# Performance work log

Hardware: AMD Instinct MI355X
Metric: run time of the kernel (lower is better)

## Reference

```python
import jax, jax.numpy as jnp
import numpy as np

B, E, H, L, V = 128, 1024, 1024, 2, 32001  # vocab = output_size + 1
PAD_IDX = 1000


def gru_cell(x, h, w_ih, w_hh, b_ih, b_hh):
    # PyTorch GRU cell math; gates ordered (r, z, n)
    gi = x @ w_ih.T + b_ih            # [B, 3H]
    gh = h @ w_hh.T + b_hh            # [B, 3H]
    i_r, i_z, i_n = jnp.split(gi, 3, axis=-1)
    h_r, h_z, h_n = jnp.split(gh, 3, axis=-1)
    r = jax.nn.sigmoid(i_r + h_r)
    z = jax.nn.sigmoid(i_z + h_z)
    n = jnp.tanh(i_n + r * h_n)
    return (1.0 - z) * n + z * h


def setup_inputs() -> dict:
    key = jax.random.key(0)
    ks = jax.random.split(key, 16)
    input_vector = jax.random.randint(ks[0], (B,), 0, V)
    hidden = jax.random.normal(ks[1], (L, B, H), dtype=jnp.float32)
    emb = jax.random.uniform(ks[2], (V, E), minval=-0.1, maxval=0.1, dtype=jnp.float32)
    emb = emb.at[PAD_IDX].set(0.0)  # padding_idx
    s = 1.0 / np.sqrt(H)
    def u(k, shape):
        return jax.random.uniform(k, shape, minval=-s, maxval=s, dtype=jnp.float32)
    w_ih0 = u(ks[3], (3 * H, E)); w_hh0 = u(ks[4], (3 * H, H))
    b_ih0 = u(ks[5], (3 * H,));  b_hh0 = u(ks[6], (3 * H,))
    w_ih1 = u(ks[7], (3 * H, H)); w_hh1 = u(ks[8], (3 * H, H))
    b_ih1 = u(ks[9], (3 * H,));  b_hh1 = u(ks[10], (3 * H,))
    w_out = jax.random.uniform(ks[11], (V, H), minval=-0.1, maxval=0.1, dtype=jnp.float32)
    b_out = jnp.zeros((V,), dtype=jnp.float32)
    return dict(input_vector=input_vector, hidden=hidden, emb=emb,
                w_ih0=w_ih0, w_hh0=w_hh0, b_ih0=b_ih0, b_hh0=b_hh0,
                w_ih1=w_ih1, w_hh1=w_hh1, b_ih1=b_ih1, b_hh1=b_hh1,
                w_out=w_out, b_out=b_out)


def reference(input_vector, hidden, emb, w_ih0, w_hh0, b_ih0, b_hh0,
              w_ih1, w_hh1, b_ih1, b_hh1, w_out, b_out):
    x = jax.nn.relu(emb[input_vector])          # [B, E] (seq_len=1 squeezed)
    h0 = gru_cell(x, hidden[0], w_ih0, w_hh0, b_ih0, b_hh0)   # [B, H]
    h1 = gru_cell(h0, hidden[1], w_ih1, w_hh1, b_ih1, b_hh1)  # [B, H]
    logits = h1 @ w_out.T + b_out               # [B, V]
    out = jax.nn.log_softmax(logits, axis=-1)   # [B, V]
    hidden_out = jnp.stack([h0, h1], axis=0)    # [L, B, H]
    return out, hidden_out
```

## Files before the change

### kernel.cpp

```cpp
#include <hip/hip_runtime.h>
#include <cmath>

#define BATCH 128
#define KDIM 1024
#define VOCAB 32001
#define G3 3072
#define GIP_STRIDE (BATCH * G3)

typedef __bf16 bf16_t;
typedef bf16_t bf16x8 __attribute__((ext_vector_type(8)));
typedef float f32x4 __attribute__((ext_vector_type(4)));

__device__ __forceinline__ void stage16(const float* g, void* lds_wave_base) {
    __builtin_amdgcn_global_load_lds(
        (const __attribute__((address_space(1))) void*)g,
        (__attribute__((address_space(3))) void*)lds_wave_base, 16, 0, 0);
}

__device__ __forceinline__ bf16x8 frag_from_lds(const float* s, int row, int quad) {
    const int s7 = row & 7;
    const f32x4 u = *(const f32x4*)(s + row * 32 + (((2 * quad) ^ s7) * 4));
    const f32x4 v = *(const f32x4*)(s + row * 32 + (((2 * quad + 1) ^ s7) * 4));
    bf16x8 r;
    r[0] = (bf16_t)u[0]; r[1] = (bf16_t)u[1]; r[2] = (bf16_t)u[2]; r[3] = (bf16_t)u[3];
    r[4] = (bf16_t)v[0]; r[5] = (bf16_t)v[1]; r[6] = (bf16_t)v[2]; r[7] = (bf16_t)v[3];
    return r;
}

template<int BM, bool BIAS>
__device__ __forceinline__ void gemm_staged_core(
    const float* __restrict__ A, const float* __restrict__ W,
    float* __restrict__ C, const float* __restrict__ bias,
    int ldc, int Wrows, int m0, int n0, int kbeg, int kend)
{
    __shared__ float sA[BM * 32];
    __shared__ float sB[64 * 32];
    const int t    = threadIdx.x;
    const int wave = t >> 6;
    const int lane = t & 63;
    const int l15  = lane & 15;
    const int quad = lane >> 4;
    const int srow = t >> 3;
    const int sg   = t & 7;

    constexpr int MFRAG = BM / 16;
    f32x4 acc[MFRAG];
#pragma unroll
    for (int i = 0; i < MFRAG; ++i) acc[i] = f32x4{0.f, 0.f, 0.f, 0.f};

    for (int k0 = kbeg; k0 < kend; k0 += 32) {
#pragma unroll
        for (int r = 0; r < BM / 32; ++r) {
            const int row = r * 32 + srow;
            const int kg  = sg ^ (row & 7);
            stage16(A + (size_t)(m0 + row) * KDIM + k0 + kg * 4,
                    (char*)sA + r * 4096 + wave * 1024);
        }
#pragma unroll
        for (int r = 0; r < 2; ++r) {
            const int row = r * 32 + srow;
            int wr = n0 + row; if (wr > Wrows - 1) wr = Wrows - 1;
            const int kg = sg ^ (row & 7);
            stage16(W + (size_t)wr * KDIM + k0 + kg * 4,
                    (char*)sB + r * 4096 + wave * 1024);
        }
        __syncthreads();
        const bf16x8 bf = frag_from_lds(sB, wave * 16 + l15, quad);
#pragma unroll
        for (int i = 0; i < MFRAG; ++i) {
            const bf16x8 af = frag_from_lds(sA, i * 16 + l15, quad);
            acc[i] = __builtin_amdgcn_mfma_f32_16x16x32_bf16(af, bf, acc[i], 0, 0, 0);
        }
        __syncthreads();
    }

    const int col = n0 + wave * 16 + l15;
    if (col < Wrows) {
        const float bv = BIAS ? bias[col] : 0.f;
#pragma unroll
        for (int i = 0; i < MFRAG; ++i)
#pragma unroll
            for (int r = 0; r < 4; ++r) {
                const int row = m0 + i * 16 + quad * 4 + r;
                C[(size_t)row * ldc + col] = acc[i][r] + bv;
            }
    }
}

__global__ __launch_bounds__(256) void gemm_vocab(const float* __restrict__ A,
                                                  const float* __restrict__ W,
                                                  const float* __restrict__ bias,
                                                  float* __restrict__ C) {
    gemm_staged_core<64, true>(A, W, C, bias, VOCAB, VOCAB,
                               blockIdx.x * 64, blockIdx.y * 64, 0, KDIM);
}

__global__ __launch_bounds__(256) void gemm_gru(const float* __restrict__ x,
                                                const float* __restrict__ wih,
                                                float* __restrict__ giP,
                                                const float* __restrict__ h,
                                                const float* __restrict__ whh,
                                                float* __restrict__ ghP) {
    const int m0    = (blockIdx.x & 1) * 64;
    const int split = blockIdx.x >> 1;
    const int n0    = blockIdx.y * 64;
    const float* A; const float* W; float* C;
    if (blockIdx.z == 0) { A = x; W = wih; C = giP; }
    else                 { A = h; W = whh; C = ghP; }
    C += (size_t)split * GIP_STRIDE;
    gemm_staged_core<64, false>(A, W, C, nullptr, G3, G3, m0, n0,
                                split * 256, split * 256 + 256);
}

__global__ __launch_bounds__(256) void embed_relu(const int* __restrict__ idx,
                                                  const float* __restrict__ emb,
                                                  float* __restrict__ x) {
    const int i  = blockIdx.x * 256 + threadIdx.x;
    const int b  = i >> 8;
    const int e4 = i & 255;
    const f32x4 v = ((const f32x4*)(emb + (size_t)idx[b] * KDIM))[e4];
    f32x4 o;
#pragma unroll
    for (int k = 0; k < 4; ++k) o[k] = fmaxf(v[k], 0.f);
    ((f32x4*)x)[i] = o;
}

__device__ __forceinline__ f32x4 sum_splits(const float* p) {
    f32x4 s = *(const f32x4*)p;
    s += *(const f32x4*)(p + GIP_STRIDE);
    s += *(const f32x4*)(p + 2 * GIP_STRIDE);
    s += *(const f32x4*)(p + 3 * GIP_STRIDE);
    return s;
}

__global__ __launch_bounds__(256) void gru_gate(const float* __restrict__ giP,
                                                const float* __restrict__ ghP,
                                                const float* __restrict__ b_ih,
                                                const float* __restrict__ b_hh,
                                                const float* __restrict__ hprev,
                                                float* __restrict__ hout) {
    const int i  = blockIdx.x * 256 + threadIdx.x;
    const int b  = i >> 8;
    const int j  = (i & 255) * 4;
    const size_t base = (size_t)b * G3 + j;

    f32x4 ir = sum_splits(giP + base),        hr = sum_splits(ghP + base);
    f32x4 iz = sum_splits(giP + base + 1024), hz = sum_splits(ghP + base + 1024);
    f32x4 in = sum_splits(giP + base + 2048), hn = sum_splits(ghP + base + 2048);
    const f32x4 bir = *(const f32x4*)(b_ih + j);
    const f32x4 biz = *(const f32x4*)(b_ih + j + 1024);
    const f32x4 bin = *(const f32x4*)(b_ih + j + 2048);
    const f32x4 bhr = *(const f32x4*)(b_hh + j);
    const f32x4 bhz = *(const f32x4*)(b_hh + j + 1024);
    const f32x4 bhn = *(const f32x4*)(b_hh + j + 2048);
    const f32x4 hp  = *(const f32x4*)(hprev + (size_t)b * KDIM + j);

    f32x4 o;
#pragma unroll
    for (int k = 0; k < 4; ++k) {
        const float r = 1.f / (1.f + __expf(-(ir[k] + bir[k] + hr[k] + bhr[k])));
        const float z = 1.f / (1.f + __expf(-(iz[k] + biz[k] + hz[k] + bhz[k])));
        const float a = in[k] + bin[k] + r * (hn[k] + bhn[k]);
        const float n = 1.f - 2.f / (__expf(2.f * a) + 1.f);
        o[k] = (1.f - z) * n + z * hp[k];
    }
    *(f32x4*)(hout + (size_t)b * KDIM + j) = o;
}

__global__ __launch_bounds__(1024) void log_softmax_rows(float* __restrict__ out) {
    float* row = out + (size_t)blockIdx.x * VOCAB;
    const int t = threadIdx.x;
    __shared__ float sm[16], ss[16];

    float m = -3.4e38f, s = 0.f;
    for (int i = t; i < VOCAB; i += 1024) {
        const float v  = row[i];
        const float mn = fmaxf(m, v);
        s = s * __expf(m - mn) + __expf(v - mn);
        m = mn;
    }
#pragma unroll
    for (int o = 32; o; o >>= 1) {
        const float mo = __shfl_down(m, o);
        const float so = __shfl_down(s, o);
        const float mn = fmaxf(m, mo);
        s = s * __expf(m - mn) + so * __expf(mo - mn);
        m = mn;
    }
    if ((t & 63) == 0) { sm[t >> 6] = m; ss[t >> 6] = s; }
    __syncthreads();
    if (t == 0) {
        float M = sm[0], S = ss[0];
#pragma unroll
        for (int w = 1; w < 16; ++w) {
            const float mn = fmaxf(M, sm[w]);
            S = S * __expf(M - mn) + ss[w] * __expf(sm[w] - mn);
            M = mn;
        }
        sm[0] = M + __logf(S);
    }
    __syncthreads();
    const float L = sm[0];

    for (int i = t * 4; i + 3 < VOCAB; i += 4096) {
        f32x4 v = *(const f32x4*)(row + i);
        v[0] -= L; v[1] -= L; v[2] -= L; v[3] -= L;
        *(f32x4*)(row + i) = v;
    }
    if (t == 0) row[32000] -= L;
}

extern "C" void kernel_launch(void* const* d_in, const int* in_sizes, int n_in,
                              void* d_out, int out_size, void* d_ws, size_t ws_size,
                              hipStream_t stream) {
    const int*   ivec  = (const int*)  d_in[0];
    const float* hidden= (const float*)d_in[1];
    const float* emb   = (const float*)d_in[2];
    const float* w_ih0 = (const float*)d_in[3];
    const float* w_hh0 = (const float*)d_in[4];
    const float* b_ih0 = (const float*)d_in[5];
    const float* b_hh0 = (const float*)d_in[6];
    const float* w_ih1 = (const float*)d_in[7];
    const float* w_hh1 = (const float*)d_in[8];
    const float* b_ih1 = (const float*)d_in[9];
    const float* b_hh1 = (const float*)d_in[10];
    const float* w_out = (const float*)d_in[11];
    const float* b_out = (const float*)d_in[12];

    float* out = (float*)d_out;
    float* h0  = out + (size_t)BATCH * VOCAB;
    float* h1  = h0 + BATCH * KDIM;

    float* x   = out;
    float* giP = out + 131072;
    float* ghP = giP + 4 * GIP_STRIDE;

    const float* hprev0 = hidden;
    const float* hprev1 = hidden + BATCH * KDIM;

    embed_relu<<<128, 256, 0, stream>>>(ivec, emb, x);

    gemm_gru<<<dim3(8, 48, 2), 256, 0, stream>>>(x, w_ih0, giP, hprev0, w_hh0, ghP);
    gru_gate<<<128, 256, 0, stream>>>(giP, ghP, b_ih0, b_hh0, hprev0, h0);

    gemm_gru<<<dim3(8, 48, 2), 256, 0, stream>>>(h0, w_ih1, giP, hprev1, w_hh1, ghP);
    gru_gate<<<128, 256, 0, stream>>>(giP, ghP, b_ih1, b_hh1, hprev1, h1);

    gemm_vocab<<<dim3(2, 501), 256, 0, stream>>>(h1, w_out, b_out, out);

    log_softmax_rows<<<128, 1024, 0, stream>>>(out);
}
```

Baseline: 349.2 us.

## Use 128-row double-buffered GEMM tiles and fuse embedding gather+ReLU into GRU GEMM

Replaces the 64-row staged GEMM with a 128x64 tile covering the whole batch, so each weight tile is loaded once instead of twice. The LDS staging is double-buffered so the next K-slice load overlaps with the MFMA work on the current one. The embedding lookup and ReLU are folded into the first GRU GEMM by gathering embedding rows directly and applying ReLU on the fragment load, which removes one kernel launch and the intermediate x buffer. The trade-off is more LDS and registers per block and half as many blocks, which lowers occupancy and parallelism.

New measurement: 358.3 us. +2.6%, slower.

```diff
diff --git a/kernel.cpp b/kernel.cpp
--- a/kernel.cpp
+++ b/kernel.cpp
@@ -17,112 +17,148 @@
         (__attribute__((address_space(3))) void*)lds_wave_base, 16, 0, 0);
 }
 
+template<bool RELU>
 __device__ __forceinline__ bf16x8 frag_from_lds(const float* s, int row, int quad) {
     const int s7 = row & 7;
-    const f32x4 u = *(const f32x4*)(s + row * 32 + (((2 * quad) ^ s7) * 4));
-    const f32x4 v = *(const f32x4*)(s + row * 32 + (((2 * quad + 1) ^ s7) * 4));
+    f32x4 u = *(const f32x4*)(s + row * 32 + (((2 * quad) ^ s7) * 4));
+    f32x4 v = *(const f32x4*)(s + row * 32 + (((2 * quad + 1) ^ s7) * 4));
+    if (RELU) {
+#pragma unroll
+        for (int k = 0; k < 4; ++k) { u[k] = fmaxf(u[k], 0.f); v[k] = fmaxf(v[k], 0.f); }
+    }
     bf16x8 r;
     r[0] = (bf16_t)u[0]; r[1] = (bf16_t)u[1]; r[2] = (bf16_t)u[2]; r[3] = (bf16_t)u[3];
     r[4] = (bf16_t)v[0]; r[5] = (bf16_t)v[1]; r[6] = (bf16_t)v[2]; r[7] = (bf16_t)v[3];
     return r;
 }
 
-template<int BM, bool BIAS>
-__device__ __forceinline__ void gemm_staged_core(
-    const float* __restrict__ A, const float* __restrict__ W,
-    float* __restrict__ C, const float* __restrict__ bias,
-    int ldc, int Wrows, int m0, int n0, int kbeg, int kend)
-{
-    __shared__ float sA[BM * 32];
-    __shared__ float sB[64 * 32];
+template<bool GATHER>
+__device__ __forceinline__ void gemm128_core(
+    const float* __restrict__ Abase, const int* __restrict__ idx,
+    const float* __restrict__ W, const float* __restrict__ bias,
+    float* __restrict__ C, int ldc, int Wrows, int n0, int kbeg, int kend)
+{
+    __shared__ float sA[2][128 * 32];
+    __shared__ float sB[2][64 * 32];
     const int t    = threadIdx.x;
     const int wave = t >> 6;
     const int lane = t & 63;
     const int l15  = lane & 15;
     const int quad = lane >> 4;
+    const int wm   = wave & 1;
+    const int wn   = wave >> 1;
     const int srow = t >> 3;
     const int sg   = t & 7;
 
-    constexpr int MFRAG = BM / 16;
-    f32x4 acc[MFRAG];
-#pragma unroll
-    for (int i = 0; i < MFRAG; ++i) acc[i] = f32x4{0.f, 0.f, 0.f, 0.f};
-
+    const float* aSrc[4];
+#pragma unroll
+    for (int r = 0; r < 4; ++r) {
+        const int row = r * 32 + srow;
+        const int kg  = sg ^ (row & 7);
+        const float* rb = GATHER ? Abase + (size_t)idx[row] * KDIM
+                                 : Abase + (size_t)row * KDIM;
+        aSrc[r] = rb + kg * 4;
+    }
+    const float* wSrc[2];
+#pragma unroll
+    for (int r = 0; r < 2; ++r) {
+        const int row = r * 32 + srow;
+        int wr = n0 + row; if (wr > Wrows - 1) wr = Wrows - 1;
+        wSrc[r] = W + (size_t)wr * KDIM + (sg ^ (row & 7)) * 4;
+    }
+
+    auto issue = [&](int k0, int buf) {
+#pragma unroll
+        for (int r = 0; r < 4; ++r)
+            stage16(aSrc[r] + k0, (char*)&sA[buf][0] + r * 4096 + wave * 1024);
+#pragma unroll
+        for (int r = 0; r < 2; ++r)
+            stage16(wSrc[r] + k0, (char*)&sB[buf][0] + r * 4096 + wave * 1024);
+    };
+
+    f32x4 acc[4][2];
+#pragma unroll
+    for (int i = 0; i < 4; ++i)
+#pragma unroll
+        for (int j = 0; j < 2; ++j) acc[i][j] = f32x4{0.f, 0.f, 0.f, 0.f};
+
+    issue(kbeg, 0);
+    __syncthreads();
+    int buf = 0;
     for (int k0 = kbeg; k0 < kend; k0 += 32) {
-#pragma unroll
-        for (int r = 0; r < BM / 32; ++r) {
-            const int row = r * 32 + srow;
-            const int kg  = sg ^ (row & 7);
-            stage16(A + (size_t)(m0 + row) * KDIM + k0 + kg * 4,
-                    (char*)sA + r * 4096 + wave * 1024);
+        if (k0 + 32 < kend) issue(k0 + 32, buf ^ 1);
+        bf16x8 bf[2];
+#pragma unroll
+        for (int j = 0; j < 2; ++j)
+            bf[j] = frag_from_lds<false>(&sB[buf][0], wn * 32 + j * 16 + l15, quad);
+#pragma unroll
+        for (int i = 0; i < 4; ++i) {
+            const bf16x8 af =
+                frag_from_lds<GATHER>(&sA[buf][0], wm * 64 + i * 16 + l15, quad);
+#pragma unroll
+            for (int j = 0; j < 2; ++j)
+                acc[i][j] = __builtin_amdgcn_mfma_f32_16x16x32_bf16(
+                    af, bf[j], acc[i][j], 0, 0, 0);
         }
-#pragma unroll
-        for (int r = 0; r < 2; ++r) {
-            const int row = r * 32 + srow;
-            int wr = n0 + row; if (wr > Wrows - 1) wr = Wrows - 1;
-            const int kg = sg ^ (row & 7);
-            stage16(W + (size_t)wr * KDIM + k0 + kg * 4,
-                    (char*)sB + r * 4096 + wave * 1024);
+        buf ^= 1;
+        __syncthreads();
+    }
+
+#pragma unroll
+    for (int j = 0; j < 2; ++j) {
+        const int col = n0 + wn * 32 + j * 16 + l15;
+        if (col < Wrows) {
+            const float bv = bias ? bias[col] : 0.f;
+#pragma unroll
+            for (int i = 0; i < 4; ++i)
+#pragma unroll
+                for (int r = 0; r < 4; ++r) {
+                    const int row = wm * 64 + i * 16 + quad * 4 + r;
+                    C[(size_t)row * ldc + col] = acc[i][j][r] + bv;
+                }
         }
-        __syncthreads();
-        const bf16x8 bf = frag_from_lds(sB, wave * 16 + l15, quad);
-#pragma unroll
-        for (int i = 0; i < MFRAG; ++i) {
-            const bf16x8 af = frag_from_lds(sA, i * 16 + l15, quad);
-            acc[i] = __builtin_amdgcn_mfma_f32_16x16x32_bf16(af, bf, acc[i], 0, 0, 0);
-        }
-        __syncthreads();
-    }
-
-    const int col = n0 + wave * 16 + l15;
-    if (col < Wrows) {
-        const float bv = BIAS ? bias[col] : 0.f;
-#pragma unroll
-        for (int i = 0; i < MFRAG; ++i)
-#pragma unroll
-            for (int r = 0; r < 4; ++r) {
-                const int row = m0 + i * 16 + quad * 4 + r;
-                C[(size_t)row * ldc + col] = acc[i][r] + bv;
-            }
-    }
-}
-
-__global__ __launch_bounds__(256) void gemm_vocab(const float* __restrict__ A,
-                                                  const float* __restrict__ W,
-                                                  const float* __restrict__ bias,
-                                                  float* __restrict__ C) {
-    gemm_staged_core<64, true>(A, W, C, bias, VOCAB, VOCAB,
-                               blockIdx.x * 64, blockIdx.y * 64, 0, KDIM);
-}
-
-__global__ __launch_bounds__(256) void gemm_gru(const float* __restrict__ x,
-                                                const float* __restrict__ wih,
-                                                float* __restrict__ giP,
-                                                const float* __restrict__ h,
-                                                const float* __restrict__ whh,
-                                                float* __restrict__ ghP) {
-    const int m0    = (blockIdx.x & 1) * 64;
-    const int split = blockIdx.x >> 1;
+    }
+}
+
+__global__ __launch_bounds__(256) void gemm_gru0(
+    const int* __restrict__ idx, const float* __restrict__ emb,
+    const float* __restrict__ wih, float* __restrict__ giP,
+    const float* __restrict__ hprev, const float* __restrict__ whh,
+    float* __restrict__ ghP)
+{
+    const int split = blockIdx.x;
     const int n0    = blockIdx.y * 64;
-    const float* A; const float* W; float* C;
-    if (blockIdx.z == 0) { A = x; W = wih; C = giP; }
-    else                 { A = h; W = whh; C = ghP; }
-    C += (size_t)split * GIP_STRIDE;
-    gemm_staged_core<64, false>(A, W, C, nullptr, G3, G3, m0, n0,
-                                split * 256, split * 256 + 256);
-}
-
-__global__ __launch_bounds__(256) void embed_relu(const int* __restrict__ idx,
-                                                  const float* __restrict__ emb,
-                                                  float* __restrict__ x) {
-    const int i  = blockIdx.x * 256 + threadIdx.x;
-    const int b  = i >> 8;
-    const int e4 = i & 255;
-    const f32x4 v = ((const f32x4*)(emb + (size_t)idx[b] * KDIM))[e4];
-    f32x4 o;
-#pragma unroll
-    for (int k = 0; k < 4; ++k) o[k] = fmaxf(v[k], 0.f);
-    ((f32x4*)x)[i] = o;
+    const int kbeg  = split * 256;
+    if (blockIdx.z == 0)
+        gemm128_core<true>(emb, idx, wih, nullptr, giP + (size_t)split * GIP_STRIDE,
+                           G3, G3, n0, kbeg, kbeg + 256);
+    else
+        gemm128_core<false>(hprev, nullptr, whh, nullptr,
+                            ghP + (size_t)split * GIP_STRIDE, G3, G3, n0, kbeg, kbeg + 256);
+}
+
+__global__ __launch_bounds__(256) void gemm_gru1(
+    const float* __restrict__ h0, const float* __restrict__ wih,
+    float* __restrict__ giP, const float* __restrict__ hprev,
+    const float* __restrict__ whh, float* __restrict__ ghP)
+{
+    const int split = blockIdx.x;
+    const int n0    = blockIdx.y * 64;
+    const int kbeg  = split * 256;
+    if (blockIdx.z == 0)
+        gemm128_core<false>(h0, nullptr, wih, nullptr,
+                            giP + (size_t)split * GIP_STRIDE, G3, G3, n0, kbeg, kbeg + 256);
+    else
+        gemm128_core<false>(hprev, nullptr, whh, nullptr,
+                            ghP + (size_t)split * GIP_STRIDE, G3, G3, n0, kbeg, kbeg + 256);
+}
+
+__global__ __launch_bounds__(256) void gemm_vocab(
+    const float* __restrict__ A, const float* __restrict__ W,
+    const float* __restrict__ bias, float* __restrict__ C)
+{
+    gemm128_core<false>(A, nullptr, W, bias, C, VOCAB, VOCAB,
+                        blockIdx.x * 64, 0, KDIM);
 }
 
 __device__ __forceinline__ f32x4 sum_splits(const float* p) {
@@ -231,22 +267,21 @@
     float* h0  = out + (size_t)BATCH * VOCAB;
     float* h1  = h0 + BATCH * KDIM;
 
-    float* x   = out;
     float* giP = out + 131072;
     float* ghP = giP + 4 * GIP_STRIDE;
 
     const float* hprev0 = hidden;
     const float* hprev1 = hidden + BATCH * KDIM;
 
-    embed_relu<<<128, 256, 0, stream>>>(ivec, emb, x);
-
-    gemm_gru<<<dim3(8, 48, 2), 256, 0, stream>>>(x, w_ih0, giP, hprev0, w_hh0, ghP);
+    gemm_gru0<<<dim3(4, 48, 2), 256, 0, stream>>>(ivec, emb, w_ih0, giP,
+                                                  hprev0, w_hh0, ghP);
     gru_gate<<<128, 256, 0, stream>>>(giP, ghP, b_ih0, b_hh0, hprev0, h0);
 
-    gemm_gru<<<dim3(8, 48, 2), 256, 0, stream>>>(h0, w_ih1, giP, hprev1, w_hh1, ghP);
+    gemm_gru1<<<dim3(4, 48, 2), 256, 0, stream>>>(h0, w_ih1, giP,
+                                                  hprev1, w_hh1, ghP);
     gru_gate<<<128, 256, 0, stream>>>(giP, ghP, b_ih1, b_hh1, hprev1, h1);
 
-    gemm_vocab<<<dim3(2, 501), 256, 0, stream>>>(h1, w_out, b_out, out);
+    gemm_vocab<<<501, 256, 0, stream>>>(h1, w_out, b_out, out);
 
     log_softmax_rows<<<128, 1024, 0, stream>>>(out);
 }
```
